# Kernel tuning notes

Measured on AMD Instinct MI355X. Metric: run time of the kernel, lower is better.

The kernel has to match this reference:

```python
import jax, jax.numpy as jnp
from jax import lax
import numpy as np

B, S, I, H, O, L = 64, 512, 1024, 1024, 1024, 2


def setup_inputs() -> dict:
    key = jax.random.key(0)
    ks = jax.random.split(key, 12)
    sI = 1.0 / np.sqrt(I)
    sH = 1.0 / np.sqrt(H)
    # weights stored as [in, out] (transpose of torch Linear.weight); same math.
    return {
        "input": jax.random.normal(ks[0], (B, S, I), jnp.float32),
        "Wxz": jax.random.uniform(ks[1], (L, I, H), jnp.float32, -sI, sI),
        "Whz": jax.random.uniform(ks[2], (L, H, H), jnp.float32, -sH, sH),
        "bz": jax.random.uniform(ks[3], (L, H), jnp.float32, -sH, sH),
        "Wxr": jax.random.uniform(ks[4], (L, I, H), jnp.float32, -sI, sI),
        "Whr": jax.random.uniform(ks[5], (L, H, H), jnp.float32, -sH, sH),
        "br": jax.random.uniform(ks[6], (L, H), jnp.float32, -sH, sH),
        "Wxg": jax.random.uniform(ks[7], (L, I, H), jnp.float32, -sI, sI),
        "Whg": jax.random.uniform(ks[8], (L, H, H), jnp.float32, -sH, sH),
        "bg": jax.random.uniform(ks[9], (L, H), jnp.float32, -sH, sH),
        "Why": jax.random.uniform(ks[10], (H, O), jnp.float32, -sH, sH),
        "by": jax.random.uniform(ks[11], (O,), jnp.float32, -sH, sH),
    }


def reference(input, Wxz, Whz, bz, Wxr, Whr, br, Wxg, Whg, bg, Why, by):
    n_layers = Whz.shape[0]
    batch = input.shape[0]
    h_dim = Whz.shape[-1]
    h0 = jnp.zeros((n_layers, batch, h_dim), input.dtype)  # (L,B,H)

    def step(h, xt):  # xt: (B,I)
        new_h = []
        inp = xt
        for l in range(n_layers):  # static, small
            hl = h[l]
            z = jax.nn.sigmoid(inp @ Wxz[l] + hl @ Whz[l] + bz[l])
            r = jax.nn.sigmoid(inp @ Wxr[l] + hl @ Whr[l] + br[l])
            g = jnp.tanh(inp @ Wxg[l] + (r * hl) @ Whg[l] + bg[l])
            hl = z * hl + (1.0 - z) * g
            new_h.append(hl)
            inp = hl
        y = inp @ Why + by  # (B,O)
        return jnp.stack(new_h), y

    hT, ys = lax.scan(step, h0, jnp.swapaxes(input, 0, 1))  # ys: (S,B,O)
    layer_output = jnp.swapaxes(ys, 0, 1)       # (B,S,O)
    hidden_state = jnp.swapaxes(hT, 0, 1)       # (B,L,H)
    return layer_output, hidden_state
```

## Files before the change

kernel.cpp:

```cpp
#include <hip/hip_runtime.h>
#include <cstdint>

using u16 = unsigned short;
using u32 = unsigned int;
using u64 = unsigned long long;

typedef __bf16 bf16x8 __attribute__((ext_vector_type(8)));
typedef float  f32x4  __attribute__((ext_vector_type(4)));
typedef unsigned int u32x4 __attribute__((ext_vector_type(4)));

#define WPITCH 2064
#define SCAN_LDS 156928
#define YG_LDS   147456
#define POLL_BOUND 32768

__device__ __forceinline__ float b2f(u16 u) {
    u32 i = ((u32)u) << 16; float f; __builtin_memcpy(&f, &i, 4); return f;
}
__device__ __forceinline__ u16 f2b(float f) {
    u32 i; __builtin_memcpy(&i, &f, 4);
    u32 r = (i + 0x7FFFu + ((i >> 16) & 1u)) >> 16; return (u16)r;
}
__device__ __forceinline__ uint4 pack8f(const float* f) {
    u16 t[8];
#pragma unroll
    for (int j = 0; j < 8; ++j) t[j] = f2b(f[j]);
    uint4 r; __builtin_memcpy(&r, t, 16); return r;
}

struct XReg { f32x4 a0, a1; u64 v0, v1; f32x4 w0, w1, w2, w3; };

__global__ __launch_bounds__(512) void gru_fused(
    const float* __restrict__ xin,
    const float* __restrict__ Wxz, const float* __restrict__ Wxr,
    const float* __restrict__ Wxg,
    const float* __restrict__ Whz, const float* __restrict__ Whr,
    const float* __restrict__ Whg,
    const float* __restrict__ bzp, const float* __restrict__ brp,
    const float* __restrict__ bgp,
    float* __restrict__ hout,
    float* __restrict__ hidden,
    u16* __restrict__ ring,
    u16* __restrict__ hb,
    u16* __restrict__ rb,
    u32* __restrict__ flags)
{
    extern __shared__ char sm[];
    char*  hs    = sm;
    char*  scZ   = sm + 33024;
    char*  xb0   = sm + 65792;
    char*  xb1   = sm + 82176;
    char*  xb2   = sm + 98560;
    char*  xb3   = sm + 114944;
    float* xls   = (float*)(sm + 131328);
    u16*   tmp16 = (u16*)(sm + 155904);

    const int tid   = threadIdx.x;
    const int lane  = tid & 63;
    const int wv    = tid >> 6;
    const int layer = blockIdx.x >> 7;
    const int id    = blockIdx.x & 127;
    const int grp   = id >> 5;
    const int w     = id & 31;
    const int bg0   = grp * 16;
    const int n0w   = w * 32;
    const long wbase = (long)layer * 1048576;
    const long bbase = (long)layer * 1024;

    u16* hbG = hb + (layer * 4 + grp) * 16384;
    u16* rbG = rb + (layer * 4 + grp) * 16384;
    u32* f_rh   = flags + ((layer * 4 + grp) * 2 + 0) * 512;
    u32* f_h    = flags + ((layer * 4 + grp) * 2 + 1) * 512;
    u32* f_h_l0 = flags + ((0 * 4 + grp) * 2 + 1) * 512;
    u32* f_h_l1 = flags + ((1 * 4 + grp) * 2 + 1) * 512;

    bf16x8 wZ[2][4], wR[2][4], wG[2][4];
#pragma unroll
    for (int nt = 0; nt < 2; ++nt) {
#pragma unroll
        for (int i = 0; i < 4; ++i) {
            const int k0  = wv * 128 + i * 32 + ((lane >> 4) << 3);
            const int col = n0w + nt * 16 + (lane & 15);
            u16 ez[8], er[8], eg[8];
#pragma unroll
            for (int j = 0; j < 8; ++j) {
                long o = wbase + (long)(k0 + j) * 1024 + col;
                ez[j] = f2b(Whz[o]); er[j] = f2b(Whr[o]); eg[j] = f2b(Whg[o]);
            }
            __builtin_memcpy(&wZ[nt][i], ez, 16);
            __builtin_memcpy(&wR[nt][i], er, 16);
            __builtin_memcpy(&wG[nt][i], eg, 16);
        }
    }

    const int b8  = tid >> 5;
    const int n32 = tid & 31;
    const int ntc = n32 >> 4, nnc = n32 & 15;
    const int ls  = ((b8 >> 2) << 4) | nnc;
    const int el  = b8 & 3;
    const float biasZ = bzp[bbase + n0w + n32];
    const float biasR = brp[bbase + n0w + n32];
    const float biasG = bgp[bbase + n0w + n32];

    f32x4 aX0 = {0,0,0,0}, aX1 = {0,0,0,0};
    const int mT0 = (wv < 6) ? 0 : 1, nT0 = (wv < 6) ? wv : wv - 6;
    const int mT1 = 1, nT1 = 2 + wv;

    auto XISSUE = [&](int kt, int wt0, XReg& X) {
        if (tid >= 256) {
            int u = tid - 256, r = u >> 3, j = u & 7;
            if (layer == 0) {
                const float* p = xin +
                    ((long)(bg0 + (r & 15)) * 512 + (wt0 + (r >> 4))) * 1024 +
                    kt * 64 + j * 8;
                X.a0 = *(const f32x4*)p;
                X.a1 = *(const f32x4*)(p + 4);
            } else {
                const u64* p = (const u64*)((const char*)ring +
                    ((long)(((wt0 + (r >> 4)) & 7) * 64 + bg0 + (r & 15)) * 1024 +
                     kt * 64 + j * 8) * 2);
                X.v0 = __hip_atomic_load(p, __ATOMIC_RELAXED,
                                         __HIP_MEMORY_SCOPE_AGENT);
                X.v1 = __hip_atomic_load(p + 1, __ATOMIC_RELAXED,
                                         __HIP_MEMORY_SCOPE_AGENT);
            }
        }
        if (tid >= 64 && tid < 448) {
            int u = tid - 64, g3 = u >> 7, rem = u & 127, k = rem >> 1,
                half = rem & 1;
            const float* Wp = (g3 == 0 ? Wxz : (g3 == 1 ? Wxr : Wxg)) + wbase +
                              (long)(kt * 64 + k) * 1024 + n0w + half * 16;
            X.w0 = *(const f32x4*)(Wp);
            X.w1 = *(const f32x4*)(Wp + 4);
            X.w2 = *(const f32x4*)(Wp + 8);
            X.w3 = *(const f32x4*)(Wp + 12);
        }
    };
    auto XSTORE = [&](char* xb, const XReg& X) {
        char* sA = xb; char* sW = xb + 4096;
        if (tid >= 256) {
            int u = tid - 256, r = u >> 3, j = u & 7;
            uint4 val;
            if (layer == 0) {
                float t[8];
                *(f32x4*)t       = X.a0;
                *(f32x4*)(t + 4) = X.a1;
                val = pack8f(t);
            } else {
                __builtin_memcpy(&val, &X.v0, 8);
                __builtin_memcpy(((char*)&val) + 8, &X.v1, 8);
            }
            *(uint4*)(sA + r * 128 + ((j * 16) ^ ((r & 7) << 4))) = val;
        }
        if (tid >= 64 && tid < 448) {
            int u = tid - 64, g3 = u >> 7, rem = u & 127, k = rem >> 1,
                half = rem & 1;
            f32x4 wv4[4] = {X.w0, X.w1, X.w2, X.w3};
#pragma unroll
            for (int c = 0; c < 16; ++c) {
                int row = g3 * 32 + half * 16 + c;
                *(u16*)(sW + row * 128 + ((k * 2) ^ ((row & 7) << 4))) =
                    f2b(wv4[c >> 2][c & 3]);
            }
        }
    };
    auto XMFMA = [&](char* xb) {
        char* sA = xb; char* sW = xb + 4096;
#pragma unroll
        for (int ks = 0; ks < 2; ++ks) {
            int kb = ks * 64 + ((lane >> 4) << 4);
            {
                int ar = mT0 * 16 + (lane & 15), br_ = nT0 * 16 + (lane & 15);
                bf16x8 aF = *(const bf16x8*)(sA + ar * 128 + (kb ^ ((ar & 7) << 4)));
                bf16x8 bF = *(const bf16x8*)(sW + br_ * 128 + (kb ^ ((br_ & 7) << 4)));
                aX0 = __builtin_amdgcn_mfma_f32_16x16x32_bf16(aF, bF, aX0, 0, 0, 0);
            }
            if (wv < 4) {
                int ar = mT1 * 16 + (lane & 15), br_ = nT1 * 16 + (lane & 15);
                bf16x8 aF = *(const bf16x8*)(sA + ar * 128 + (kb ^ ((ar & 7) << 4)));
                bf16x8 bF = *(const bf16x8*)(sW + br_ * 128 + (kb ^ ((br_ & 7) << 4)));
                aX1 = __builtin_amdgcn_mfma_f32_16x16x32_bf16(aF, bF, aX1, 0, 0, 0);
            }
        }
    };
    auto XP4 = [&](int kt0, int wt0, XReg& A, XReg& B, int nkt, int nwt0,
                   bool dn) {
        XSTORE(xb0, A);
        XSTORE(xb1, B);
        XISSUE(kt0 + 2, wt0, A);
        XISSUE(kt0 + 3, wt0, B);
        __syncthreads();
        XMFMA(xb0);
        XMFMA(xb1);
        XSTORE(xb2, A);
        XSTORE(xb3, B);
        if (dn) { XISSUE(nkt, nwt0, A); XISSUE(nkt + 1, nwt0, B); }
        __syncthreads();
        XMFMA(xb2);
        XMFMA(xb3);
    };
    auto XWRITE = [&](int buf) {
#pragma unroll
        for (int q = 0; q < 4; ++q) {
            int row = mT0 * 16 + ((lane >> 4) << 2) + q;
            xls[((buf * 2 + mT0) * 16 + (row & 15)) * 96 + nT0 * 16 + (lane & 15)] = aX0[q];
            if (wv < 4) {
                int row1 = 16 + ((lane >> 4) << 2) + q;
                xls[((buf * 2 + 1) * 16 + (row1 & 15)) * 96 + nT1 * 16 + (lane & 15)] = aX1[q];
            }
        }
        aX0 = (f32x4){0,0,0,0}; aX1 = (f32x4){0,0,0,0};
    };
    auto STAGE32 = [&](const char* src) {
        u32x4 a0, a1, a2, a3;
        const char* p = src + tid * 16;
        asm volatile(
            "global_load_dwordx4 %0, %4, off sc0 sc1\n\t"
            "global_load_dwordx4 %1, %5, off sc0 sc1\n\t"
            "global_load_dwordx4 %2, %6, off sc0 sc1\n\t"
            "global_load_dwordx4 %3, %7, off sc0 sc1\n\t"
            "s_waitcnt vmcnt(0)"
            : "=&v"(a0), "=&v"(a1), "=&v"(a2), "=&v"(a3)
            : "v"(p), "v"(p + 8192), "v"(p + 16384), "v"(p + 24576)
            : "memory");
        u32x4 a[4] = {a0, a1, a2, a3};
#pragma unroll
        for (int u = 0; u < 4; ++u) {
            int idx = u * 512 + tid;
            *(u32x4*)(hs + (idx >> 7) * WPITCH +
                      (((idx & 127) * 16) ^ (((idx >> 7) & 7) << 4))) = a[u];
        }
    };
    auto PUBLISH = [&](char* dst) {
        if (tid < 64) {
            int b = tid >> 2, q = tid & 3;
            u16 e[8];
#pragma unroll
            for (int j = 0; j < 8; ++j) e[j] = tmp16[b * 32 + q * 8 + j];
            u32x4 v; __builtin_memcpy(&v, e, 16);
            char* p = dst + b * 2048 + n0w * 2 + q * 16;
            asm volatile("global_store_dwordx4 %0, %1, off sc0 sc1"
                         :: "v"(p), "v"(v) : "memory");
        }
    };
    auto FLAGREL = [&](u32* fp, u32 tgtv) {
        if (tid == 0)
            asm volatile("s_waitcnt vmcnt(0)\n\t"
                         "global_store_dword %0, %1, off sc0 sc1"
                         :: "v"(fp), "v"(tgtv) : "memory");
    };
    auto FLAGWAIT = [&](const u32* fpbase, u32 tgtv) {
        if (tid < 32) {
            const u32* fp = fpbase + tid * 16;
            u32 v; int itc = 0;
            for (;;) {
                asm volatile("global_load_dword %0, %1, off sc0 sc1\n\t"
                             "s_waitcnt vmcnt(0)"
                             : "=v"(v) : "v"(fp) : "memory");
                if (v >= tgtv) break;
                if (++itc > POLL_BOUND) break;
                __builtin_amdgcn_s_sleep(1);
            }
        }
        __builtin_amdgcn_sched_barrier(0);
        __syncthreads();
    };

    XReg A, B;
    {
        if (layer == 1) FLAGWAIT(f_h_l0, 4);
        XISSUE(0, 0, A);
        XISSUE(1, 0, B);
        XP4(0, 0, A, B, 4, 0, true);
        XP4(4, 0, A, B, 8, 0, true);
        XP4(8, 0, A, B, 12, 0, true);
        XP4(12, 0, A, B, 0, 2, true);
        __syncthreads();
        XWRITE(0);
        __syncthreads();
    }

    float h_own = 0.f;
    for (int tc = 0; tc < 512; ++tc) {
        const bool prod = (tc < 510);
        const int wt0 = (tc & ~1) + 2;
        const int kb8 = (tc & 1) * 8;
        const int buf = (tc >> 1) & 1;
        const int tl  = tc & 1;

        if (layer == 0 && tc >= 8)
            FLAGWAIT(f_h_l1, (u32)(tc - 8));

        if (prod) XP4(kb8 + 0, wt0, A, B, -1, -1, false);

        if (tc == 0) {
            __syncthreads();
#pragma unroll
            for (int u = 0; u < 4; ++u) {
                int idx = u * 512 + tid;
                *(u32x4*)(hs + (idx >> 7) * WPITCH +
                          (((idx & 127) * 16) ^ (((idx >> 7) & 7) << 4))) =
                    (u32x4){0, 0, 0, 0};
            }
        } else {
            FLAGWAIT(f_h, (u32)tc);
            if (layer == 0)
                STAGE32((const char*)ring + (((tc - 1) & 7) * 64 + bg0) * 2048);
            else
                STAGE32((const char*)hbG);
        }
        __syncthreads();

        {
            f32x4 aZ0 = {0,0,0,0}, aZ1 = {0,0,0,0};
            f32x4 aR0 = {0,0,0,0}, aR1 = {0,0,0,0};
#pragma unroll
            for (int i = 0; i < 4; ++i) {
                int kby = wv * 256 + i * 64 + ((lane >> 4) << 4);
                int ar = lane & 15;
                bf16x8 aF = *(const bf16x8*)(hs + ar * WPITCH + (kby ^ ((ar & 7) << 4)));
                aZ0 = __builtin_amdgcn_mfma_f32_16x16x32_bf16(aF, wZ[0][i], aZ0, 0, 0, 0);
                aZ1 = __builtin_amdgcn_mfma_f32_16x16x32_bf16(aF, wZ[1][i], aZ1, 0, 0, 0);
                aR0 = __builtin_amdgcn_mfma_f32_16x16x32_bf16(aF, wR[0][i], aR0, 0, 0, 0);
                aR1 = __builtin_amdgcn_mfma_f32_16x16x32_bf16(aF, wR[1][i], aR1, 0, 0, 0);
            }
            *(f32x4*)(scZ + ((0 * 8 + wv) * 64 + lane) * 16) = aZ0;
            *(f32x4*)(scZ + ((1 * 8 + wv) * 64 + lane) * 16) = aZ1;
            *(f32x4*)(scZ + ((2 * 8 + wv) * 64 + lane) * 16) = aR0;
            *(f32x4*)(scZ + ((3 * 8 + wv) * 64 + lane) * 16) = aR1;
        }
        __syncthreads();

        float zval;
        {
            float sz = 0.f, sr = 0.f;
#pragma unroll
            for (int ww = 0; ww < 8; ++ww) {
                sz += *(const float*)(scZ + (((ntc)     * 8 + ww) * 64 + ls) * 16 + el * 4);
                sr += *(const float*)(scZ + (((2 + ntc) * 8 + ww) * 64 + ls) * 16 + el * 4);
            }
            const float* xrow = xls + ((buf * 2 + tl) * 16 + b8) * 96;
            sz += xrow[n32] + biasZ;
            sr += xrow[32 + n32] + biasR;
            zval = 1.f / (1.f + __expf(-sz));
            float rv = 1.f / (1.f + __expf(-sr));
            tmp16[b8 * 32 + n32] = f2b(rv * h_own);
        }
        __syncthreads();

        PUBLISH((char*)rbG);
        FLAGREL(f_rh + w * 16, (u32)(tc + 1));

        if (prod) {
            const bool dn  = (tc + 1 < 510);
            if (layer == 1 && tl == 1 && dn)
                FLAGWAIT(f_h_l0, (u32)(tc + 5));
            XISSUE(kb8 + 4, wt0, A);
            XISSUE(kb8 + 5, wt0, B);
            const int nkb  = ((tc + 1) & 1) * 8;
            const int nwt  = ((tc + 1) & ~1) + 2;
            XP4(kb8 + 4, wt0, A, B, nkb, nwt, dn);
        }

        FLAGWAIT(f_rh, (u32)(tc + 1));
        STAGE32((const char*)rbG);
        __syncthreads();

        {
            f32x4 aG0 = {0,0,0,0}, aG1 = {0,0,0,0};
#pragma unroll
            for (int i = 0; i < 4; ++i) {
                int kby = wv * 256 + i * 64 + ((lane >> 4) << 4);
                int ar = lane & 15;
                bf16x8 aF = *(const bf16x8*)(hs + ar * WPITCH + (kby ^ ((ar & 7) << 4)));
                aG0 = __builtin_amdgcn_mfma_f32_16x16x32_bf16(aF, wG[0][i], aG0, 0, 0, 0);
                aG1 = __builtin_amdgcn_mfma_f32_16x16x32_bf16(aF, wG[1][i], aG1, 0, 0, 0);
            }
            *(f32x4*)(scZ + ((0 * 8 + wv) * 64 + lane) * 16) = aG0;
            *(f32x4*)(scZ + ((1 * 8 + wv) * 64 + lane) * 16) = aG1;
        }
        __syncthreads();

        {
            float sg = 0.f;
#pragma unroll
            for (int ww = 0; ww < 8; ++ww)
                sg += *(const float*)(scZ + ((ntc * 8 + ww) * 64 + ls) * 16 + el * 4);
            sg += xls[((buf * 2 + tl) * 16 + b8) * 96 + 64 + n32] + biasG;
            float e  = __expf(-2.f * sg);
            float gt = 2.f / (1.f + e) - 1.f;
            float hn = zval * h_own + (1.f - zval) * gt;
            h_own = hn;
            tmp16[b8 * 32 + n32] = f2b(hn);
            if (layer == 1)
                hout[((long)(bg0 + b8) * 512 + tc) * 1024 + n0w + n32] = hn;
            if (tc == 511)
                hidden[(long)(bg0 + b8) * 2048 + layer * 1024 + n0w + n32] = hn;
        }
        __syncthreads();

        PUBLISH(layer == 0
                    ? (char*)ring + (((tc & 7) * 64 + bg0) * 2048)
                    : (char*)hbG);
        FLAGREL(f_h + w * 16, (u32)(tc + 1));

        if (tl == 1 && prod) {
            __syncthreads();
            XWRITE(buf ^ 1);
        }
    }
}

__global__ __launch_bounds__(256) void ygemm(const float* __restrict__ Why,
                                             const float* __restrict__ by,
                                             float* __restrict__ y)
{
    extern __shared__ char sm[];
    char* sA = sm;
    char* sW = sm + 131072;

    const int tid  = threadIdx.x;
    const int lane = tid & 63;
    const int wv   = tid >> 6;
    const long r0  = (long)blockIdx.x * 64;

    for (int it = 0; it < 32; ++it) {
        int c = it * 256 + tid;
        int row = c >> 7, j = c & 127;
        long gi = (r0 + row) * 1024 + j * 8;
        float tp[8];
        *(uint4*)tp       = *(const uint4*)(y + gi);
        *(uint4*)(tp + 4) = *(const uint4*)(y + gi + 4);
        *(uint4*)(sA + row * 2048 + ((j * 16) ^ ((row & 7) << 4))) = pack8f(tp);
    }
    __syncthreads();

    for (int nt = 0; nt < 8; ++nt) {
        f32x4 acc[4][2] = {};
        for (int kt = 0; kt < 16; ++kt) {
            __syncthreads();
#pragma unroll
            for (int uu = 0; uu < 4; ++uu) {
                int u = uu * 256 + tid;
                int nrow = u >> 3, jc = u & 7;
                u16 e[8];
#pragma unroll
                for (int q = 0; q < 8; ++q)
                    e[q] = f2b(Why[(long)(kt * 64 + jc * 8 + q) * 1024 + nt * 128 + nrow]);
                uint4 v; __builtin_memcpy(&v, e, 16);
                *(uint4*)(sW + nrow * 128 + ((jc * 16) ^ ((nrow & 7) << 4))) = v;
            }
            __syncthreads();
#pragma unroll
            for (int ks = 0; ks < 2; ++ks) {
                int kbA = kt * 128 + ks * 64 + ((lane >> 4) << 4);
                int kbW = ks * 64 + ((lane >> 4) << 4);
#pragma unroll
                for (int cc = 0; cc < 2; ++cc) {
                    int brr = (wv * 2 + cc) * 16 + (lane & 15);
                    bf16x8 bF = *(const bf16x8*)(sW + brr * 128 + (kbW ^ ((brr & 7) << 4)));
#pragma unroll
                    for (int m = 0; m < 4; ++m) {
                        int ar = m * 16 + (lane & 15);
                        bf16x8 aF = *(const bf16x8*)(sA + ar * 2048 + (kbA ^ ((ar & 7) << 4)));
                        acc[m][cc] = __builtin_amdgcn_mfma_f32_16x16x32_bf16(
                            aF, bF, acc[m][cc], 0, 0, 0);
                    }
                }
            }
        }
#pragma unroll
        for (int cc = 0; cc < 2; ++cc) {
            int col = nt * 128 + (wv * 2 + cc) * 16 + (lane & 15);
            float bv = by[col];
#pragma unroll
            for (int m = 0; m < 4; ++m)
#pragma unroll
                for (int q = 0; q < 4; ++q) {
                    long row = r0 + m * 16 + ((lane >> 4) << 2) + q;
                    y[row * 1024 + col] = acc[m][cc][q] + bv;
                }
        }
    }
}

extern "C" void kernel_launch(void* const* d_in, const int* in_sizes, int n_in,
                              void* d_out, int out_size, void* d_ws,
                              size_t ws_size, hipStream_t stream) {
    const float* input = (const float*)d_in[0];
    const float* Wxz = (const float*)d_in[1];
    const float* Whz = (const float*)d_in[2];
    const float* bz  = (const float*)d_in[3];
    const float* Wxr = (const float*)d_in[4];
    const float* Whr = (const float*)d_in[5];
    const float* br  = (const float*)d_in[6];
    const float* Wxg = (const float*)d_in[7];
    const float* Whg = (const float*)d_in[8];
    const float* bg  = (const float*)d_in[9];
    const float* Why = (const float*)d_in[10];
    const float* by  = (const float*)d_in[11];
    (void)in_sizes; (void)n_in; (void)out_size; (void)ws_size;

    float* yreg   = (float*)d_out;
    float* hidden = yreg + 33554432;

    char* ws = (char*)d_ws;
    u32* flags = (u32*)ws;
    u16* hb    = (u16*)(ws + 32768);
    u16* rb    = (u16*)(ws + 294912);
    u16* ring  = (u16*)(ws + 557056);

    hipFuncSetAttribute(reinterpret_cast<const void*>(gru_fused),
                        hipFuncAttributeMaxDynamicSharedMemorySize, SCAN_LDS);
    hipFuncSetAttribute(reinterpret_cast<const void*>(ygemm),
                        hipFuncAttributeMaxDynamicSharedMemorySize, YG_LDS);
    hipMemsetAsync(flags, 0, 32768, stream);

    gru_fused<<<256, 512, SCAN_LDS, stream>>>(
        input, Wxz, Wxr, Wxg, Whz, Whr, Whg, bz, br, bg,
        yreg, hidden, ring, hb, rb, flags);
    ygemm<<<512, 256, YG_LDS, stream>>>(Why, by, yreg);
}
```

Before: 11.98 ms.

## Use per-wave flag polling and staging to drop block barriers in the recurrent step

Each wave now polls only the four producer flags covering its own 256-byte column slice of the hidden state, loads just that slice, and writes it into its own LDS region. That removes the block-wide FLAGWAIT and two __syncthreads per half-step, so waves can start their MFMAs as soon as their own inputs arrive. The risk is correctness: it assumes the flag-to-column mapping matches the layout, and that no other wave reads the LDS rows being overwritten. It also drops the tc==0 barrier, which relies on the same per-wave ownership.

```diff
diff --git a/kernel.cpp b/kernel.cpp
--- a/kernel.cpp
+++ b/kernel.cpp
@@ -211,9 +211,26 @@
         }
         aX0 = (f32x4){0,0,0,0}; aX1 = (f32x4){0,0,0,0};
     };
-    auto STAGE32 = [&](const char* src) {
+    auto WVSTAGE = [&](const u32* fpbase, u32 tgtv, const char* src) {
+        if (lane < 4) {
+            const u32* fp = fpbase + (wv * 4 + lane) * 16;
+            u32 v; int itc = 0;
+            for (;;) {
+                asm volatile("global_load_dword %0, %1, off sc0 sc1\n\t"
+                             "s_waitcnt vmcnt(0)"
+                             : "=v"(v) : "v"(fp) : "memory");
+                if (v >= tgtv) break;
+                if (++itc > POLL_BOUND) break;
+                __builtin_amdgcn_s_sleep(1);
+            }
+        }
+        __builtin_amdgcn_sched_barrier(0);
+        const int colb = wv * 256 + (lane & 15) * 16;
+        const char* p0 = src + (long)(lane >> 4) * 2048 + colb;
+        const char* p1 = p0 + 4 * 2048;
+        const char* p2 = p0 + 8 * 2048;
+        const char* p3 = p0 + 12 * 2048;
         u32x4 a0, a1, a2, a3;
-        const char* p = src + tid * 16;
         asm volatile(
             "global_load_dwordx4 %0, %4, off sc0 sc1\n\t"
             "global_load_dwordx4 %1, %5, off sc0 sc1\n\t"
@@ -221,15 +238,13 @@
             "global_load_dwordx4 %3, %7, off sc0 sc1\n\t"
             "s_waitcnt vmcnt(0)"
             : "=&v"(a0), "=&v"(a1), "=&v"(a2), "=&v"(a3)
-            : "v"(p), "v"(p + 8192), "v"(p + 16384), "v"(p + 24576)
+            : "v"(p0), "v"(p1), "v"(p2), "v"(p3)
             : "memory");
-        u32x4 a[4] = {a0, a1, a2, a3};
-#pragma unroll
-        for (int u = 0; u < 4; ++u) {
-            int idx = u * 512 + tid;
-            *(u32x4*)(hs + (idx >> 7) * WPITCH +
-                      (((idx & 127) * 16) ^ (((idx >> 7) & 7) << 4))) = a[u];
-        }
+        int b = lane >> 4;
+        *(u32x4*)(hs + b * WPITCH + (colb ^ ((b & 7) << 4))) = a0; b += 4;
+        *(u32x4*)(hs + b * WPITCH + (colb ^ ((b & 7) << 4))) = a1; b += 4;
+        *(u32x4*)(hs + b * WPITCH + (colb ^ ((b & 7) << 4))) = a2; b += 4;
+        *(u32x4*)(hs + b * WPITCH + (colb ^ ((b & 7) << 4))) = a3;
     };
     auto PUBLISH = [&](char* dst) {
         if (tid < 64) {
@@ -294,22 +309,19 @@
         if (prod) XP4(kb8 + 0, wt0, A, B, -1, -1, false);
 
         if (tc == 0) {
-            __syncthreads();
-#pragma unroll
-            for (int u = 0; u < 4; ++u) {
-                int idx = u * 512 + tid;
-                *(u32x4*)(hs + (idx >> 7) * WPITCH +
-                          (((idx & 127) * 16) ^ (((idx >> 7) & 7) << 4))) =
+            const int colb = wv * 256 + (lane & 15) * 16;
+#pragma unroll
+            for (int ld = 0; ld < 4; ++ld) {
+                int b = ld * 4 + (lane >> 4);
+                *(u32x4*)(hs + b * WPITCH + (colb ^ ((b & 7) << 4))) =
                     (u32x4){0, 0, 0, 0};
             }
         } else {
-            FLAGWAIT(f_h, (u32)tc);
-            if (layer == 0)
-                STAGE32((const char*)ring + (((tc - 1) & 7) * 64 + bg0) * 2048);
-            else
-                STAGE32((const char*)hbG);
-        }
-        __syncthreads();
+            WVSTAGE(f_h, (u32)tc,
+                    (layer == 0)
+                        ? (const char*)ring + (((tc - 1) & 7) * 64 + bg0) * 2048
+                        : (const char*)hbG);
+        }
 
         {
             f32x4 aZ0 = {0,0,0,0}, aZ1 = {0,0,0,0};
@@ -362,9 +374,7 @@
             XP4(kb8 + 4, wt0, A, B, nkb, nwt, dn);
         }
 
-        FLAGWAIT(f_rh, (u32)(tc + 1));
-        STAGE32((const char*)rbG);
-        __syncthreads();
+        WVSTAGE(f_rh, (u32)(tc + 1), (const char*)rbG);
 
         {
             f32x4 aG0 = {0,0,0,0}, aG1 = {0,0,0,0};
```

New measurement: 14.13 ms. +18.0%, slower.
